# Kernel optimization log

Hardware: AMD Instinct MI355X
Metric: run time of the kernel (lower is better)

Reference implementation:

```python
import jax, jax.numpy as jnp
import numpy as np

S, B, F = 2048, 16, 100
E, H, NOUT, DEC, FF, NH = 512, 512, 10, 1024, 2048, 8
DH = E // NH


def _ln(h, g, b):
    m = h.mean(-1, keepdims=True)
    v = ((h - m) ** 2).mean(-1, keepdims=True)
    return (h - m) * jax.lax.rsqrt(v + 1e-5) * g + b


def setup_inputs() -> dict:
    key = jax.random.key(0)
    ks = jax.random.split(key, 24)
    w = lambda k, shp, s=0.02: (jax.random.normal(k, shp, dtype=jnp.float32) * s)
    return {
        "x": jax.random.normal(ks[0], (S, B, F), dtype=jnp.float32),
        "y": jax.random.normal(ks[1], (S, B), dtype=jnp.float32),
        "enc_W": w(ks[2], (F, E), 0.1), "enc_b": jnp.zeros((E,), jnp.float32),
        "yenc_W": w(ks[3], (1, E), 0.1), "yenc_b": jnp.zeros((E,), jnp.float32),
        "Wq": w(ks[4], (E, E)), "Wk": w(ks[5], (E, E)),
        "Wv": w(ks[6], (E, E)), "Wo": w(ks[7], (E, E)),
        "ln1_g": jnp.ones((E,), jnp.float32), "ln1_b": jnp.zeros((E,), jnp.float32),
        "ln2_g": jnp.ones((E,), jnp.float32), "ln2_b": jnp.zeros((E,), jnp.float32),
        "ffn_W1": w(ks[8], (E, FF)), "ffn_b1": jnp.zeros((FF,), jnp.float32),
        "ffn_W2": w(ks[9], (FF, E)), "ffn_b2": jnp.zeros((E,), jnp.float32),
        "dec_W": w(ks[10], (E, DEC)), "dec_b": jnp.zeros((DEC,), jnp.float32),
        "head_w1_W": w(ks[11], (DEC, F * H)),
        "head_b1_W": w(ks[12], (DEC, H)),
        "head_w2_W": w(ks[13], (DEC, H * NOUT)),
        "head_b2_W": w(ks[14], (DEC, NOUT)),
        "single_eval_pos": 1024,
    }


def reference(x, y, enc_W, enc_b, yenc_W, yenc_b, Wq, Wk, Wv, Wo,
              ln1_g, ln1_b, ln2_g, ln2_b, ffn_W1, ffn_b1, ffn_W2, ffn_b2,
              dec_W, dec_b, head_w1_W, head_b1_W, head_w2_W, head_b2_W,
              single_eval_pos):
    sep = int(single_eval_pos)
    # encoders
    x_src = x @ enc_W + enc_b                       # [S,B,E]
    y_src = y[..., None] @ yenc_W + yenc_b          # [S,B,E]
    train_x = x_src[:sep] + y_src[:sep]             # [T,B,E]

    # inner_forward: one post-LN transformer encoder layer over train tokens
    q = (train_x @ Wq).reshape(sep, B, NH, DH)
    k = (train_x @ Wk).reshape(sep, B, NH, DH)
    v = (train_x @ Wv).reshape(sep, B, NH, DH)
    scores = jnp.einsum('tbhd,sbhd->bhts', q, k) / np.sqrt(DH).astype(np.float32)
    attn = jax.nn.softmax(scores, axis=-1)
    ao = jnp.einsum('bhts,sbhd->tbhd', attn, v).reshape(sep, B, E) @ Wo
    z = _ln(train_x + ao, ln1_g, ln1_b)
    ff = jax.nn.relu(z @ ffn_W1 + ffn_b1) @ ffn_W2 + ffn_b2
    out = _ln(z + ff, ln2_g, ln2_b)                 # [T,B,E]

    # decoder: mean-pool over train tokens, emit per-batch MLP weights
    pooled = out.mean(0)                            # [B,E]
    dh = jax.nn.relu(pooled @ dec_W + dec_b)        # [B,DEC]
    w1 = (dh @ head_w1_W).reshape(B, F, H)
    b1 = dh @ head_b1_W                             # [B,H]
    w2 = (dh @ head_w2_W).reshape(B, H, NOUT)
    b2 = dh @ head_b2_W                             # [B,NOUT]

    # per-batch generated MLP on eval tokens (no_double_embedding path)
    x_eval = jnp.nan_to_num(x[sep:])                # [Eval,B,F]
    h = jnp.einsum('ebf,bfh->ebh', x_eval, w1) + b1
    h = jax.nn.relu(h)
    h = jnp.einsum('ebh,bho->ebo', h, w2) + b2
    return h                                        # [Eval,B,NOUT]
```

## Files before the change

### kernel.cpp

```cpp
#include <hip/hip_runtime.h>
#include <math.h>

#define SEP   1024
#define EVALN 1024
#define BB    16
#define FIN   100
#define FINP  128
#define EE    512
#define NHH   8
#define DHH   64
#define FFNN  2048
#define DECN  1024
#define HHN   512
#define NOUTN 10
#define TBR   (SEP * BB)
#define MB    (1024u * 1024u)

typedef short  s16x8 __attribute__((ext_vector_type(8)));
typedef float  f32x4 __attribute__((ext_vector_type(4)));

__device__ __forceinline__ unsigned short f2b(float f) {
  union { float f; unsigned int u; } v; v.f = f;
  unsigned int u = v.u;
  return (unsigned short)((u + 0x7fffu + ((u >> 16) & 1u)) >> 16);
}

__device__ __forceinline__ float nan2num(float v) {
  if (isnan(v)) return 0.f;
  if (isinf(v)) return v > 0.f ? 3.4028234663852886e38f : -3.4028234663852886e38f;
  return v;
}

__device__ __forceinline__ void gld16(const void* g, void* l) {
  __builtin_amdgcn_global_load_lds(
      (const __attribute__((address_space(1))) unsigned int*)g,
      (__attribute__((address_space(3))) unsigned int*)l, 16, 0, 0);
}

__global__ __launch_bounds__(256)
void transcast(const float* __restrict__ W, unsigned short* __restrict__ Wt,
               int K, int N, int Kp) {
  __shared__ float t[32][33];
  const int n0 = blockIdx.x * 32, k0 = blockIdx.y * 32;
  const int tx = threadIdx.x, ty = threadIdx.y;
#pragma unroll
  for (int r = 0; r < 4; ++r) {
    const int k = k0 + ty + r * 8;
    t[ty + r * 8][tx] = (k < K) ? W[(size_t)k * N + n0 + tx] : 0.f;
  }
  __syncthreads();
#pragma unroll
  for (int r = 0; r < 4; ++r) {
    const int n = n0 + ty + r * 8;
    Wt[(size_t)n * Kp + k0 + tx] = f2b(t[tx][ty + r * 8]);
  }
}

__global__ __launch_bounds__(256)
void castx_kernel(const float* __restrict__ x, unsigned short* __restrict__ xb) {
  const int idx = blockIdx.x * 256 + threadIdx.x;
  const int m = idx >> 7, f = idx & 127;
  xb[idx] = (f < FIN) ? f2b(x[(size_t)m * FIN + f]) : (unsigned short)0;
}

template <bool YENC, bool BIAS, bool RELU, bool OF32, bool OB16>
__global__ __launch_bounds__(256)
void gemm_bf16(const unsigned short* __restrict__ A,
               const unsigned short* __restrict__ Bt,
               float* __restrict__ C32, unsigned short* __restrict__ C16,
               const float* __restrict__ bias, const float* __restrict__ yb2,
               const float* __restrict__ yvec, const float* __restrict__ yW,
               int M, int N, int K) {
  __shared__ unsigned short As[128 * 32];
  __shared__ unsigned short Bs[128 * 32];
  const int tid = threadIdx.x;
  const int wave = tid >> 6, lane = tid & 63;
  const int q = lane >> 4, c = lane & 15;
  const int wm = wave >> 1, wn = wave & 1;
  const int m0 = blockIdx.y * 128, n0 = blockIdx.x * 128;
  const int srow = lane >> 2;
  const int qlog = (lane & 3) ^ (lane >> 4);
  const int rA0 = wave * 32 + srow;
  const int rA1 = rA0 + 16;
  unsigned short* lA0 = As + wave * 1024;
  unsigned short* lA1 = As + wave * 1024 + 512;
  unsigned short* lB0 = Bs + wave * 1024;
  unsigned short* lB1 = Bs + wave * 1024 + 512;
  const unsigned short* gA0 = A + (size_t)(m0 + rA0) * K + qlog * 8;
  const unsigned short* gA1 = A + (size_t)(m0 + rA1) * K + qlog * 8;
  const unsigned short* gB0 = Bt + (size_t)(n0 + rA0) * K + qlog * 8;
  const unsigned short* gB1 = Bt + (size_t)(n0 + rA1) * K + qlog * 8;

  f32x4 acc[4][4];
#pragma unroll
  for (int i = 0; i < 4; ++i)
#pragma unroll
    for (int j = 0; j < 4; ++j) acc[i][j] = (f32x4){0.f, 0.f, 0.f, 0.f};

  const int pchunk = (q ^ (c >> 2)) * 8;
  const int aoff = (wm * 64 + c) * 32 + pchunk;
  const int boff = (wn * 64 + c) * 32 + pchunk;

  for (int k0 = 0; k0 < K; k0 += 32) {
    gld16(gA0 + k0, lA0);
    gld16(gA1 + k0, lA1);
    gld16(gB0 + k0, lB0);
    gld16(gB1 + k0, lB1);
    __syncthreads();
    s16x8 af[4], bf[4];
#pragma unroll
    for (int mi = 0; mi < 4; ++mi)
      af[mi] = *(const s16x8*)&As[aoff + mi * 16 * 32];
#pragma unroll
    for (int ni = 0; ni < 4; ++ni)
      bf[ni] = *(const s16x8*)&Bs[boff + ni * 16 * 32];
#pragma unroll
    for (int mi = 0; mi < 4; ++mi)
#pragma unroll
      for (int ni = 0; ni < 4; ++ni)
        acc[mi][ni] = __builtin_amdgcn_mfma_f32_16x16x32_bf16(
            af[mi], bf[ni], acc[mi][ni], 0, 0, 0);
    __syncthreads();
  }

  float bb[4], yw[4];
#pragma unroll
  for (int ni = 0; ni < 4; ++ni) {
    const int n = n0 + wn * 64 + ni * 16 + c;
    float t = 0.f;
    if (BIAS) t = bias[n];
    if (YENC) t = bias[n] + yb2[n];
    bb[ni] = t;
    yw[ni] = YENC ? yW[n] : 0.f;
  }
#pragma unroll
  for (int mi = 0; mi < 4; ++mi) {
#pragma unroll
    for (int r = 0; r < 4; ++r) {
      const int m = m0 + wm * 64 + mi * 16 + q * 4 + r;
      const float yv = YENC ? yvec[m] : 0.f;
#pragma unroll
      for (int ni = 0; ni < 4; ++ni) {
        const int n = n0 + wn * 64 + ni * 16 + c;
        float val = acc[mi][ni][r] + bb[ni];
        if (YENC) val = fmaf(yv, yw[ni], val);
        if (RELU) val = fmaxf(val, 0.f);
        if (OF32) C32[(size_t)m * N + n] = val;
        if (OB16) C16[(size_t)m * N + n] = f2b(val);
      }
    }
  }
}

__global__ __launch_bounds__(256)
void vtrans(const unsigned short* __restrict__ qkv, unsigned short* __restrict__ vt) {
  __shared__ unsigned short t[64][72];
  const int s0 = blockIdx.x * 64;
  const int h = blockIdx.y, b = blockIdx.z;
  const int tid = threadIdx.x;
  const int r = tid >> 2, o = (tid & 3) * 16;
  const unsigned short* g =
      qkv + ((size_t)(s0 + r) * BB + b) * 1536 + 1024 + h * 64 + o;
  unsigned short tmp[16];
  *(uint4*)tmp = *(const uint4*)g;
  *(uint4*)(tmp + 8) = *(const uint4*)(g + 8);
#pragma unroll
  for (int i = 0; i < 16; ++i) t[o + i][r] = tmp[i];
  __syncthreads();
  unsigned short tmp2[16];
#pragma unroll
  for (int i = 0; i < 16; ++i) {
    const int p = o + i;
    tmp2[i] = t[r][16 * (p & 3) + (p >> 2)];
  }
  unsigned short* out =
      vt + ((size_t)(b * NHH + h) * 64 + r) * 1024 + s0 + o;
  *(uint4*)out = *(const uint4*)&tmp2[0];
  *(uint4*)(out + 8) = *(const uint4*)&tmp2[8];
}

__global__ __launch_bounds__(256)
void attn_mfma(const unsigned short* __restrict__ qkv,
               const unsigned short* __restrict__ vt,
               unsigned short* __restrict__ aob) {
  __shared__ unsigned short Qs[64][72];
  __shared__ unsigned short Ks[64][72];
  __shared__ unsigned short Vts[64][72];
  __shared__ unsigned short Pls[4][16][72];
  const int tid = threadIdx.x;
  const int w = tid >> 6, lane = tid & 63;
  const int q = lane >> 4, c = lane & 15;
  const int hb = blockIdx.x;
  const int h = hb & (NHH - 1), b = hb >> 3;
  const int t0 = blockIdx.y * 64;
  const int bh = b * NHH + h;
  const int sr = tid >> 2, so = (tid & 3) * 16;

  {
    const unsigned short* g =
        qkv + ((size_t)(t0 + sr) * BB + b) * 1536 + h * 64 + so;
    *(uint4*)&Qs[sr][so] = *(const uint4*)g;
    *(uint4*)&Qs[sr][so + 8] = *(const uint4*)(g + 8);
  }
  __syncthreads();
  s16x8 aq[2];
  aq[0] = *(const s16x8*)&Qs[w * 16 + c][q * 8];
  aq[1] = *(const s16x8*)&Qs[w * 16 + c][32 + q * 8];

  float m_s[4], l_s[4];
  f32x4 oacc[4];
#pragma unroll
  for (int r = 0; r < 4; ++r) { m_s[r] = -3.0e38f; l_s[r] = 0.f; }
#pragma unroll
  for (int dt = 0; dt < 4; ++dt) oacc[dt] = (f32x4){0.f, 0.f, 0.f, 0.f};

  uint4 kr0, kr1, vr0, vr1;
  {
    const unsigned short* gk =
        qkv + ((size_t)sr * BB + b) * 1536 + 512 + h * 64 + so;
    kr0 = *(const uint4*)gk; kr1 = *(const uint4*)(gk + 8);
    const unsigned short* gv = vt + ((size_t)bh * 64 + sr) * 1024 + so;
    vr0 = *(const uint4*)gv; vr1 = *(const uint4*)(gv + 8);
  }
  *(uint4*)&Ks[sr][so] = kr0; *(uint4*)&Ks[sr][so + 8] = kr1;
  *(uint4*)&Vts[sr][so] = vr0; *(uint4*)&Vts[sr][so + 8] = vr1;
  __syncthreads();

  for (int s0 = 0; s0 < SEP; s0 += 64) {
    const bool more = (s0 + 64 < SEP);
    if (more) {
      const unsigned short* gk =
          qkv + ((size_t)(s0 + 64 + sr) * BB + b) * 1536 + 512 + h * 64 + so;
      kr0 = *(const uint4*)gk; kr1 = *(const uint4*)(gk + 8);
      const unsigned short* gv =
          vt + ((size_t)bh * 64 + sr) * 1024 + s0 + 64 + so;
      vr0 = *(const uint4*)gv; vr1 = *(const uint4*)(gv + 8);
    }
    f32x4 sacc[4];
#pragma unroll
    for (int ch = 0; ch < 4; ++ch) sacc[ch] = (f32x4){0.f, 0.f, 0.f, 0.f};
#pragma unroll
    for (int ch = 0; ch < 4; ++ch) {
#pragma unroll
      for (int kh = 0; kh < 2; ++kh) {
        s16x8 bk = *(const s16x8*)&Ks[ch * 16 + c][kh * 32 + q * 8];
        sacc[ch] = __builtin_amdgcn_mfma_f32_16x16x32_bf16(
            aq[kh], bk, sacc[ch], 0, 0, 0);
      }
    }
    float rmax[4];
#pragma unroll
    for (int r = 0; r < 4; ++r) {
      float mx = -3.0e38f;
#pragma unroll
      for (int ch = 0; ch < 4; ++ch) mx = fmaxf(mx, sacc[ch][r] * 0.125f);
      rmax[r] = mx;
    }
#pragma unroll
    for (int mask = 1; mask < 16; mask <<= 1)
#pragma unroll
      for (int r = 0; r < 4; ++r)
        rmax[r] = fmaxf(rmax[r], __shfl_xor(rmax[r], mask));
    float alpha[4], rsum[4];
    float p[4][4];
#pragma unroll
    for (int r = 0; r < 4; ++r) {
      const float mnew = fmaxf(m_s[r], rmax[r]);
      alpha[r] = __expf(m_s[r] - mnew);
      float sum = 0.f;
#pragma unroll
      for (int ch = 0; ch < 4; ++ch) {
        const float pv = __expf(sacc[ch][r] * 0.125f - mnew);
        p[ch][r] = pv;
        sum += pv;
      }
      rsum[r] = sum;
      m_s[r] = mnew;
    }
#pragma unroll
    for (int mask = 1; mask < 16; mask <<= 1)
#pragma unroll
      for (int r = 0; r < 4; ++r) rsum[r] += __shfl_xor(rsum[r], mask);
#pragma unroll
    for (int r = 0; r < 4; ++r) l_s[r] = l_s[r] * alpha[r] + rsum[r];
#pragma unroll
    for (int dt = 0; dt < 4; ++dt)
#pragma unroll
      for (int r = 0; r < 4; ++r) oacc[dt][r] *= alpha[r];
#pragma unroll
    for (int r = 0; r < 4; ++r) {
      uint2 pk;
      pk.x = (unsigned)f2b(p[0][r]) | ((unsigned)f2b(p[1][r]) << 16);
      pk.y = (unsigned)f2b(p[2][r]) | ((unsigned)f2b(p[3][r]) << 16);
      *(uint2*)&Pls[w][q * 4 + r][c * 4] = pk;
    }
#pragma unroll
    for (int kh = 0; kh < 2; ++kh) {
      s16x8 ap = *(const s16x8*)&Pls[w][c][kh * 32 + q * 8];
#pragma unroll
      for (int dt = 0; dt < 4; ++dt) {
        s16x8 bv = *(const s16x8*)&Vts[dt * 16 + c][kh * 32 + q * 8];
        oacc[dt] = __builtin_amdgcn_mfma_f32_16x16x32_bf16(
            ap, bv, oacc[dt], 0, 0, 0);
      }
    }
    __syncthreads();
    if (more) {
      *(uint4*)&Ks[sr][so] = kr0; *(uint4*)&Ks[sr][so + 8] = kr1;
      *(uint4*)&Vts[sr][so] = vr0; *(uint4*)&Vts[sr][so + 8] = vr1;
      __syncthreads();
    }
  }
  float inv[4];
#pragma unroll
  for (int r = 0; r < 4; ++r) inv[r] = 1.f / l_s[r];
#pragma unroll
  for (int dt = 0; dt < 4; ++dt) {
#pragma unroll
    for (int r = 0; r < 4; ++r) {
      const int m = t0 + w * 16 + q * 4 + r;
      aob[((size_t)m * BB + b) * EE + h * 64 + dt * 16 + c] =
          f2b(oacc[dt][r] * inv[r]);
    }
  }
}

template <bool B16>
__global__ __launch_bounds__(256)
void ln_k(const float* __restrict__ a, const float* __restrict__ r_,
          const float* __restrict__ g, const float* __restrict__ be,
          float* __restrict__ o32, unsigned short* __restrict__ o16) {
  __shared__ float ss[4], sqs[4];
  const int row = blockIdx.x;
  const int tid = threadIdx.x;
  const size_t base = (size_t)row * EE;
  const float x0 = a[base + tid] + r_[base + tid];
  const float x1 = a[base + tid + 256] + r_[base + tid + 256];
  float s = x0 + x1;
  float sq = x0 * x0 + x1 * x1;
#pragma unroll
  for (int off = 32; off >= 1; off >>= 1) {
    s += __shfl_xor(s, off);
    sq += __shfl_xor(sq, off);
  }
  const int wid = tid >> 6;
  if ((tid & 63) == 0) { ss[wid] = s; sqs[wid] = sq; }
  __syncthreads();
  s = ss[0] + ss[1] + ss[2] + ss[3];
  sq = sqs[0] + sqs[1] + sqs[2] + sqs[3];
  const float mean = s * (1.f / 512.f);
  const float var = sq * (1.f / 512.f) - mean * mean;
  const float rstd = rsqrtf(fmaxf(var, 0.f) + 1e-5f);
  const float v0 = (x0 - mean) * rstd * g[tid] + be[tid];
  const float v1 = (x1 - mean) * rstd * g[tid + 256] + be[tid + 256];
  o32[base + tid] = v0;
  o32[base + tid + 256] = v1;
  if (B16) {
    o16[base + tid] = f2b(v0);
    o16[base + tid + 256] = f2b(v1);
  }
}

__global__ __launch_bounds__(256)
void pool1(const float* __restrict__ outb, float* __restrict__ pp) {
  const int i = blockIdx.x * 256 + threadIdx.x;
  const int ts = blockIdx.y;
  const float* p = outb + (size_t)ts * 64 * (BB * EE) + i;
  float s0 = 0.f, s1 = 0.f, s2 = 0.f, s3 = 0.f;
  for (int t = 0; t < 64; t += 4) {
    s0 += p[(size_t)(t + 0) * (BB * EE)];
    s1 += p[(size_t)(t + 1) * (BB * EE)];
    s2 += p[(size_t)(t + 2) * (BB * EE)];
    s3 += p[(size_t)(t + 3) * (BB * EE)];
  }
  pp[ts * (BB * EE) + i] = (s0 + s1) + (s2 + s3);
}

__global__ __launch_bounds__(256)
void pool2(const float* __restrict__ pp, float* __restrict__ pooled) {
  const int i = blockIdx.x * 256 + threadIdx.x;
  float s = 0.f;
#pragma unroll
  for (int ts = 0; ts < 16; ++ts) s += pp[ts * (BB * EE) + i];
  pooled[i] = s * (1.f / (float)SEP);
}

__global__ __launch_bounds__(256)
void dec1(const float* __restrict__ pooled, const float* __restrict__ dW,
          float* __restrict__ pd) {
  __shared__ float ps[128];
  const int ks = blockIdx.x, b = blockIdx.y;
  const int tid = threadIdx.x;
  if (tid < 128) ps[tid] = pooled[b * EE + ks * 128 + tid];
  __syncthreads();
  const int n = tid * 4;
  float4 acc = {0.f, 0.f, 0.f, 0.f};
  for (int kk = 0; kk < 128; kk += 4) {
    const float4 p4 = *(const float4*)&ps[kk];
#pragma unroll
    for (int i = 0; i < 4; ++i) {
      const float4 w4 = *(const float4*)&dW[(size_t)(ks * 128 + kk + i) * DECN + n];
      const float pv = (i == 0) ? p4.x : (i == 1) ? p4.y : (i == 2) ? p4.z : p4.w;
      acc.x = fmaf(pv, w4.x, acc.x); acc.y = fmaf(pv, w4.y, acc.y);
      acc.z = fmaf(pv, w4.z, acc.z); acc.w = fmaf(pv, w4.w, acc.w);
    }
  }
  *(float4*)&pd[(size_t)(ks * BB + b) * DECN + n] = acc;
}

__global__ __launch_bounds__(256)
void dec2(const float* __restrict__ pd, const float* __restrict__ db,
          float* __restrict__ dh) {
  const int idx = blockIdx.x * 256 + threadIdx.x;
  const int b = idx >> 10, n = idx & 1023;
  float s = db[n];
#pragma unroll
  for (int ks = 0; ks < 4; ++ks) s += pd[(size_t)(ks * BB + b) * DECN + n];
  dh[idx] = fmaxf(s, 0.f);
}

template <int KL>
__global__ __launch_bounds__(256)
void hgemm_split(const float* __restrict__ dh, const float* __restrict__ W,
                 float* __restrict__ part, int N) {
  __shared__ float dhs[16][KL];
  const int tid = threadIdx.x;
  const int n0 = blockIdx.x * 1024;
  const int k0 = blockIdx.y * KL;
  for (int i = tid; i < 16 * (KL / 4); i += 256) {
    const int b = i / (KL / 4), kq = i % (KL / 4);
    *(float4*)&dhs[b][kq * 4] = *(const float4*)&dh[b * DECN + k0 + kq * 4];
  }
  __syncthreads();
  float* pb = part + (size_t)blockIdx.y * 16 * N;
  if ((N & 3) == 0) {
    const int n = n0 + tid * 4;
    if (n + 3 < N) {
      float4 acc[16];
#pragma unroll
      for (int b = 0; b < 16; ++b) acc[b] = (float4){0.f, 0.f, 0.f, 0.f};
      for (int kk = 0; kk < KL; kk += 4) {
        float4 w4[4];
#pragma unroll
        for (int i = 0; i < 4; ++i)
          w4[i] = *(const float4*)&W[(size_t)(k0 + kk + i) * N + n];
#pragma unroll
        for (int b = 0; b < 16; ++b) {
          const float4 d4 = *(const float4*)&dhs[b][kk];
          acc[b].x = fmaf(d4.x, w4[0].x, acc[b].x);
          acc[b].y = fmaf(d4.x, w4[0].y, acc[b].y);
          acc[b].z = fmaf(d4.x, w4[0].z, acc[b].z);
          acc[b].w = fmaf(d4.x, w4[0].w, acc[b].w);
          acc[b].x = fmaf(d4.y, w4[1].x, acc[b].x);
          acc[b].y = fmaf(d4.y, w4[1].y, acc[b].y);
          acc[b].z = fmaf(d4.y, w4[1].z, acc[b].z);
          acc[b].w = fmaf(d4.y, w4[1].w, acc[b].w);
          acc[b].x = fmaf(d4.z, w4[2].x, acc[b].x);
          acc[b].y = fmaf(d4.z, w4[2].y, acc[b].y);
          acc[b].z = fmaf(d4.z, w4[2].z, acc[b].z);
          acc[b].w = fmaf(d4.z, w4[2].w, acc[b].w);
          acc[b].x = fmaf(d4.w, w4[3].x, acc[b].x);
          acc[b].y = fmaf(d4.w, w4[3].y, acc[b].y);
          acc[b].z = fmaf(d4.w, w4[3].z, acc[b].z);
          acc[b].w = fmaf(d4.w, w4[3].w, acc[b].w);
        }
      }
#pragma unroll
      for (int b = 0; b < 16; ++b) *(float4*)&pb[(size_t)b * N + n] = acc[b];
    }
  } else {
    const int n = n0 + tid;
    if (n < N) {
      float acc[16];
#pragma unroll
      for (int b = 0; b < 16; ++b) acc[b] = 0.f;
      for (int kk = 0; kk < KL; ++kk) {
        const float w = W[(size_t)(k0 + kk) * N + n];
#pragma unroll
        for (int b = 0; b < 16; ++b) acc[b] = fmaf(dhs[b][kk], w, acc[b]);
      }
#pragma unroll
      for (int b = 0; b < 16; ++b) pb[(size_t)b * N + n] = acc[b];
    }
  }
}

__global__ __launch_bounds__(256)
void hg_reduce(const float* __restrict__ part, float* __restrict__ out,
               int total, int S) {
  const int i4 = (blockIdx.x * 256 + threadIdx.x) * 4;
  if (i4 >= total) return;
  float4 s = *(const float4*)&part[i4];
  for (int p = 1; p < S; ++p) {
    const float4 v = *(const float4*)&part[(size_t)p * total + i4];
    s.x += v.x; s.y += v.y; s.z += v.z; s.w += v.w;
  }
  *(float4*)&out[i4] = s;
}

__global__ __launch_bounds__(256)
void eval1_kernel(const float* __restrict__ x, const float* __restrict__ w1,
                  const float* __restrict__ b1, float* __restrict__ h1) {
  __shared__ float xs[8][100];
  const int b = blockIdx.z;
  const int e0 = blockIdx.y << 3;
  const int hcol = blockIdx.x * 256 + threadIdx.x;
  for (int i = threadIdx.x; i < 800; i += 256) {
    const int ee = i / 100, f = i - ee * 100;
    xs[ee][f] = nan2num(x[((size_t)(SEP + e0 + ee) * BB + b) * FIN + f]);
  }
  __syncthreads();
  float acc[8];
#pragma unroll
  for (int i = 0; i < 8; ++i) acc[i] = 0.f;
  for (int f = 0; f < FIN; ++f) {
    const float w = w1[(size_t)b * (FIN * HHN) + (size_t)f * HHN + hcol];
#pragma unroll
    for (int ee = 0; ee < 8; ++ee) acc[ee] = fmaf(xs[ee][f], w, acc[ee]);
  }
  const float bias = b1[b * HHN + hcol];
#pragma unroll
  for (int ee = 0; ee < 8; ++ee)
    h1[((size_t)(e0 + ee) * BB + b) * HHN + hcol] = fmaxf(acc[ee] + bias, 0.f);
}

__global__ __launch_bounds__(256)
void eval2_kernel(const float* __restrict__ h1, const float* __restrict__ w2,
                  const float* __restrict__ b2, float* __restrict__ outp) {
  __shared__ float w2s[10][512];
  __shared__ float red[4][64][10];
  const int b = blockIdx.y;
  const int e0 = blockIdx.x * 64;
  const int tid = threadIdx.x;
  const int r = tid & 63, ks = tid >> 6;
  for (int i = tid; i < 5120; i += 256) {
    const int o = i >> 9, k = i & 511;
    w2s[o][k] = w2[(size_t)b * (HHN * NOUTN) + k * NOUTN + o];
  }
  __syncthreads();
  const int eb = (e0 + r) * BB + b;
  const float* hp = h1 + (size_t)eb * HHN + ks * 128;
  float acc[10];
#pragma unroll
  for (int o = 0; o < 10; ++o) acc[o] = 0.f;
  for (int kk = 0; kk < 128; kk += 4) {
    const float4 h4 = *(const float4*)&hp[kk];
#pragma unroll
    for (int o = 0; o < 10; ++o) {
      const float4 w4 = *(const float4*)&w2s[o][ks * 128 + kk];
      acc[o] = fmaf(h4.x, w4.x, acc[o]);
      acc[o] = fmaf(h4.y, w4.y, acc[o]);
      acc[o] = fmaf(h4.z, w4.z, acc[o]);
      acc[o] = fmaf(h4.w, w4.w, acc[o]);
    }
  }
#pragma unroll
  for (int o = 0; o < 10; ++o) red[ks][r][o] = acc[o];
  __syncthreads();
  if (ks == 0) {
#pragma unroll
    for (int o = 0; o < 10; ++o)
      outp[(size_t)eb * NOUTN + o] = red[0][r][o] + red[1][r][o] +
                                     red[2][r][o] + red[3][r][o] +
                                     b2[b * NOUTN + o];
  }
}

extern "C" void kernel_launch(void* const* d_in, const int* in_sizes, int n_in,
                              void* d_out, int out_size, void* d_ws, size_t ws_size,
                              hipStream_t stream) {
  const float* x      = (const float*)d_in[0];
  const float* y      = (const float*)d_in[1];
  const float* enc_W  = (const float*)d_in[2];
  const float* enc_b  = (const float*)d_in[3];
  const float* yenc_W = (const float*)d_in[4];
  const float* yenc_b = (const float*)d_in[5];
  const float* Wq     = (const float*)d_in[6];
  const float* Wk     = (const float*)d_in[7];
  const float* Wv     = (const float*)d_in[8];
  const float* Wo     = (const float*)d_in[9];
  const float* ln1_g  = (const float*)d_in[10];
  const float* ln1_b  = (const float*)d_in[11];
  const float* ln2_g  = (const float*)d_in[12];
  const float* ln2_b  = (const float*)d_in[13];
  const float* ffn_W1 = (const float*)d_in[14];
  const float* ffn_b1 = (const float*)d_in[15];
  const float* ffn_W2 = (const float*)d_in[16];
  const float* ffn_b2 = (const float*)d_in[17];
  const float* dec_W  = (const float*)d_in[18];
  const float* dec_b  = (const float*)d_in[19];
  const float* hw1    = (const float*)d_in[20];
  const float* hb1    = (const float*)d_in[21];
  const float* hw2    = (const float*)d_in[22];
  const float* hb2    = (const float*)d_in[23];

  char* ws = (char*)d_ws;
  unsigned short* ff1b  = (unsigned short*)(ws + 0 * MB);
  unsigned short* xb    = (unsigned short*)(ws + 0 * MB);
  float*          pp    = (float*)(ws + 0 * MB);
  float*          pd    = (float*)(ws + 1 * MB);
  float*          hgp   = (float*)(ws + 2 * MB);
  unsigned short* txb   = (unsigned short*)(ws + 16 * MB);
  unsigned short* vt    = (unsigned short*)(ws + 32 * MB);
  unsigned short* aob   = (unsigned short*)(ws + 48 * MB);
  unsigned short* qkvb  = (unsigned short*)(ws + 64 * MB);
  float*          z32   = (float*)(ws + 64 * MB);
  unsigned short* zb    = (unsigned short*)(ws + 96 * MB);
  float*          tx32  = (float*)(ws + 112 * MB);
  float*          ff2   = (float*)(ws + 112 * MB);
  float*          aop   = (float*)(ws + 144 * MB);
  float*          outb  = (float*)(ws + 144 * MB);
  float*          h1    = (float*)(ws + 144 * MB);
  size_t wo_ = 176 * (size_t)MB;
  unsigned short* WencT = (unsigned short*)(ws + wo_); wo_ += (size_t)EE * FINP * 2;
  unsigned short* WqkvT = (unsigned short*)(ws + wo_); wo_ += (size_t)3 * EE * EE * 2;
  unsigned short* WoT   = (unsigned short*)(ws + wo_); wo_ += (size_t)EE * EE * 2;
  unsigned short* W1T   = (unsigned short*)(ws + wo_); wo_ += (size_t)FFNN * EE * 2;
  unsigned short* W2T   = (unsigned short*)(ws + wo_); wo_ += (size_t)EE * FFNN * 2;
  float* pooled = (float*)(ws + wo_); wo_ += (size_t)BB * EE * 4;
  float* dh     = (float*)(ws + wo_); wo_ += (size_t)BB * DECN * 4;
  float* w1g    = (float*)(ws + wo_); wo_ += (size_t)BB * FIN * HHN * 4;
  float* b1g    = (float*)(ws + wo_); wo_ += (size_t)BB * HHN * 4;
  float* w2g    = (float*)(ws + wo_); wo_ += (size_t)BB * HHN * NOUTN * 4;
  float* b2g    = (float*)(ws + wo_);
  float* outp = (float*)d_out;

  transcast<<<dim3(EE / 32, FINP / 32), dim3(32, 8), 0, stream>>>(enc_W, WencT, FIN, EE, FINP);
  transcast<<<dim3(EE / 32, EE / 32), dim3(32, 8), 0, stream>>>(Wq, WqkvT, EE, EE, EE);
  transcast<<<dim3(EE / 32, EE / 32), dim3(32, 8), 0, stream>>>(Wk, WqkvT + (size_t)EE * EE, EE, EE, EE);
  transcast<<<dim3(EE / 32, EE / 32), dim3(32, 8), 0, stream>>>(Wv, WqkvT + (size_t)2 * EE * EE, EE, EE, EE);
  transcast<<<dim3(EE / 32, EE / 32), dim3(32, 8), 0, stream>>>(Wo, WoT, EE, EE, EE);
  transcast<<<dim3(FFNN / 32, EE / 32), dim3(32, 8), 0, stream>>>(ffn_W1, W1T, EE, FFNN, EE);
  transcast<<<dim3(EE / 32, FFNN / 32), dim3(32, 8), 0, stream>>>(ffn_W2, W2T, FFNN, EE, FFNN);
  castx_kernel<<<(TBR * FINP) / 256, 256, 0, stream>>>(x, xb);

  gemm_bf16<true, false, false, true, true><<<dim3(EE / 128, TBR / 128), 256, 0, stream>>>(
      xb, WencT, tx32, txb, enc_b, yenc_b, y, yenc_W, TBR, EE, FINP);
  gemm_bf16<false, false, false, false, true><<<dim3(1536 / 128, TBR / 128), 256, 0, stream>>>(
      txb, WqkvT, nullptr, qkvb, nullptr, nullptr, nullptr, nullptr, TBR, 1536, EE);
  vtrans<<<dim3(SEP / 64, NHH, BB), 256, 0, stream>>>(qkvb, vt);
  attn_mfma<<<dim3(NHH * BB, SEP / 64), 256, 0, stream>>>(qkvb, vt, aob);
  gemm_bf16<false, false, false, true, false><<<dim3(EE / 128, TBR / 128), 256, 0, stream>>>(
      aob, WoT, aop, nullptr, nullptr, nullptr, nullptr, nullptr, TBR, EE, EE);
  ln_k<true><<<TBR, 256, 0, stream>>>(tx32, aop, ln1_g, ln1_b, z32, zb);
  gemm_bf16<false, true, true, false, true><<<dim3(FFNN / 128, TBR / 128), 256, 0, stream>>>(
      zb, W1T, nullptr, ff1b, ffn_b1, nullptr, nullptr, nullptr, TBR, FFNN, EE);
  gemm_bf16<false, true, false, true, false><<<dim3(EE / 128, TBR / 128), 256, 0, stream>>>(
      ff1b, W2T, ff2, nullptr, ffn_b2, nullptr, nullptr, nullptr, TBR, EE, FFNN);
  ln_k<false><<<TBR, 256, 0, stream>>>(z32, ff2, ln2_g, ln2_b, outb, nullptr);
  pool1<<<dim3(32, 16), 256, 0, stream>>>(outb, pp);
  pool2<<<32, 256, 0, stream>>>(pp, pooled);
  dec1<<<dim3(4, BB), 256, 0, stream>>>(pooled, dec_W, pd);
  dec2<<<64, 256, 0, stream>>>(pd, dec_b, dh);
  hgemm_split<128><<<dim3(50, 8), 256, 0, stream>>>(dh, hw1, hgp, FIN * HHN);
  hg_reduce<<<800, 256, 0, stream>>>(hgp, w1g, BB * FIN * HHN, 8);
  hgemm_split<64><<<dim3(5, 16), 256, 0, stream>>>(dh, hw2, hgp, HHN * NOUTN);
  hg_reduce<<<80, 256, 0, stream>>>(hgp, w2g, BB * HHN * NOUTN, 16);
  hgemm_split<64><<<dim3(1, 16), 256, 0, stream>>>(dh, hb1, hgp, HHN);
  hg_reduce<<<8, 256, 0, stream>>>(hgp, b1g, BB * HHN, 16);
  hgemm_split<64><<<dim3(1, 16), 256, 0, stream>>>(dh, hb2, hgp, NOUTN);
  hg_reduce<<<1, 256, 0, stream>>>(hgp, b2g, BB * NOUTN, 16);
  eval1_kernel<<<dim3(HHN / 256, EVALN / 8, BB), 256, 0, stream>>>(x, w1g, b1g, h1);
  eval2_kernel<<<dim3(EVALN / 64, BB), 256, 0, stream>>>(h1, w2g, b2g, outp);
}
```

Measured before the change: 853.8 us.

## Fuse prep, decoder, small heads and eval kernels; add MFMA priority hints

Merges the eight weight-transpose and input-cast launches into a single prep kernel, and fuses pool2/dec1/dec2 into one decoder kernel. It replaces the b1/b2 head split-GEMMs with one small_heads kernel and fuses the two eval MLP stages so the hidden activations stay in shared memory. It also wraps the attention MFMA blocks with s_setprio. The aim is to cut kernel launch count and intermediate global traffic. The trade-off is less parallelism in some fused kernels, such as dec_fused reading all of K serially and eval_fused using only 160 active threads in its second stage.

Result: no change. 852.8 us (-0.1%).

```diff
diff --git a/kernel.cpp b/kernel.cpp
--- a/kernel.cpp
+++ b/kernel.cpp
@@ -38,29 +38,54 @@
 }
 
 __global__ __launch_bounds__(256)
-void transcast(const float* __restrict__ W, unsigned short* __restrict__ Wt,
-               int K, int N, int Kp) {
-  __shared__ float t[32][33];
-  const int n0 = blockIdx.x * 32, k0 = blockIdx.y * 32;
-  const int tx = threadIdx.x, ty = threadIdx.y;
+void prep_fused(const float* __restrict__ x,
+                const float* __restrict__ enc_W, const float* __restrict__ Wq,
+                const float* __restrict__ Wk, const float* __restrict__ Wv,
+                const float* __restrict__ Wo, const float* __restrict__ W1,
+                const float* __restrict__ W2,
+                unsigned short* __restrict__ xb, unsigned short* __restrict__ WencT,
+                unsigned short* __restrict__ WqkvT, unsigned short* __restrict__ WoT,
+                unsigned short* __restrict__ W1T, unsigned short* __restrict__ W2T) {
+  const int bid = blockIdx.x;
+  const int tid = threadIdx.x;
+  if (bid < 8192) {
+    const int idx = bid * 256 + tid;
+    const int m = idx >> 7, f = idx & 127;
+    xb[idx] = (f < FIN) ? f2b(x[(size_t)m * FIN + f]) : (unsigned short)0;
+    return;
+  }
+  int t = bid - 8192;
+  const float* W; unsigned short* Wt; int K, N, Kp, gx;
+  if (t < 64) {
+    W = enc_W; Wt = WencT; K = FIN; N = EE; Kp = FINP; gx = 16;
+  } else if ((t -= 64) < 256) {
+    W = Wq; Wt = WqkvT; K = EE; N = EE; Kp = EE; gx = 16;
+  } else if ((t -= 256) < 256) {
+    W = Wk; Wt = WqkvT + (size_t)EE * EE; K = EE; N = EE; Kp = EE; gx = 16;
+  } else if ((t -= 256) < 256) {
+    W = Wv; Wt = WqkvT + (size_t)2 * EE * EE; K = EE; N = EE; Kp = EE; gx = 16;
+  } else if ((t -= 256) < 256) {
+    W = Wo; Wt = WoT; K = EE; N = EE; Kp = EE; gx = 16;
+  } else if ((t -= 256) < 1024) {
+    W = W1; Wt = W1T; K = EE; N = FFNN; Kp = EE; gx = 64;
+  } else {
+    t -= 1024;
+    W = W2; Wt = W2T; K = FFNN; N = EE; Kp = FFNN; gx = 16;
+  }
+  __shared__ float tb[32][33];
+  const int n0 = (t % gx) * 32, k0 = (t / gx) * 32;
+  const int tx = tid & 31, ty = tid >> 5;
 #pragma unroll
   for (int r = 0; r < 4; ++r) {
     const int k = k0 + ty + r * 8;
-    t[ty + r * 8][tx] = (k < K) ? W[(size_t)k * N + n0 + tx] : 0.f;
+    tb[ty + r * 8][tx] = (k < K) ? W[(size_t)k * N + n0 + tx] : 0.f;
   }
   __syncthreads();
 #pragma unroll
   for (int r = 0; r < 4; ++r) {
     const int n = n0 + ty + r * 8;
-    Wt[(size_t)n * Kp + k0 + tx] = f2b(t[tx][ty + r * 8]);
-  }
-}
-
-__global__ __launch_bounds__(256)
-void castx_kernel(const float* __restrict__ x, unsigned short* __restrict__ xb) {
-  const int idx = blockIdx.x * 256 + threadIdx.x;
-  const int m = idx >> 7, f = idx & 127;
-  xb[idx] = (f < FIN) ? f2b(x[(size_t)m * FIN + f]) : (unsigned short)0;
+    Wt[(size_t)n * Kp + k0 + tx] = f2b(tb[tx][ty + r * 8]);
+  }
 }
 
 template <bool YENC, bool BIAS, bool RELU, bool OF32, bool OB16>
@@ -239,6 +264,7 @@
     f32x4 sacc[4];
 #pragma unroll
     for (int ch = 0; ch < 4; ++ch) sacc[ch] = (f32x4){0.f, 0.f, 0.f, 0.f};
+    __builtin_amdgcn_s_setprio(1);
 #pragma unroll
     for (int ch = 0; ch < 4; ++ch) {
 #pragma unroll
@@ -248,6 +274,7 @@
             aq[kh], bk, sacc[ch], 0, 0, 0);
       }
     }
+    __builtin_amdgcn_s_setprio(0);
     float rmax[4];
 #pragma unroll
     for (int r = 0; r < 4; ++r) {
@@ -294,6 +321,7 @@
       pk.y = (unsigned)f2b(p[2][r]) | ((unsigned)f2b(p[3][r]) << 16);
       *(uint2*)&Pls[w][q * 4 + r][c * 4] = pk;
     }
+    __builtin_amdgcn_s_setprio(1);
 #pragma unroll
     for (int kh = 0; kh < 2; ++kh) {
       s16x8 ap = *(const s16x8*)&Pls[w][c][kh * 32 + q * 8];
@@ -304,6 +332,7 @@
             ap, bv, oacc[dt], 0, 0, 0);
       }
     }
+    __builtin_amdgcn_s_setprio(0);
     __syncthreads();
     if (more) {
       *(uint4*)&Ks[sr][so] = kr0; *(uint4*)&Ks[sr][so + 8] = kr1;
@@ -377,46 +406,27 @@
 }
 
 __global__ __launch_bounds__(256)
-void pool2(const float* __restrict__ pp, float* __restrict__ pooled) {
-  const int i = blockIdx.x * 256 + threadIdx.x;
-  float s = 0.f;
-#pragma unroll
-  for (int ts = 0; ts < 16; ++ts) s += pp[ts * (BB * EE) + i];
-  pooled[i] = s * (1.f / (float)SEP);
-}
-
-__global__ __launch_bounds__(256)
-void dec1(const float* __restrict__ pooled, const float* __restrict__ dW,
-          float* __restrict__ pd) {
-  __shared__ float ps[128];
-  const int ks = blockIdx.x, b = blockIdx.y;
-  const int tid = threadIdx.x;
-  if (tid < 128) ps[tid] = pooled[b * EE + ks * 128 + tid];
-  __syncthreads();
-  const int n = tid * 4;
-  float4 acc = {0.f, 0.f, 0.f, 0.f};
-  for (int kk = 0; kk < 128; kk += 4) {
-    const float4 p4 = *(const float4*)&ps[kk];
-#pragma unroll
-    for (int i = 0; i < 4; ++i) {
-      const float4 w4 = *(const float4*)&dW[(size_t)(ks * 128 + kk + i) * DECN + n];
-      const float pv = (i == 0) ? p4.x : (i == 1) ? p4.y : (i == 2) ? p4.z : p4.w;
-      acc.x = fmaf(pv, w4.x, acc.x); acc.y = fmaf(pv, w4.y, acc.y);
-      acc.z = fmaf(pv, w4.z, acc.z); acc.w = fmaf(pv, w4.w, acc.w);
-    }
-  }
-  *(float4*)&pd[(size_t)(ks * BB + b) * DECN + n] = acc;
-}
-
-__global__ __launch_bounds__(256)
-void dec2(const float* __restrict__ pd, const float* __restrict__ db,
-          float* __restrict__ dh) {
-  const int idx = blockIdx.x * 256 + threadIdx.x;
-  const int b = idx >> 10, n = idx & 1023;
-  float s = db[n];
-#pragma unroll
-  for (int ks = 0; ks < 4; ++ks) s += pd[(size_t)(ks * BB + b) * DECN + n];
-  dh[idx] = fmaxf(s, 0.f);
+void dec_fused(const float* __restrict__ pp, const float* __restrict__ dW,
+               const float* __restrict__ db, float* __restrict__ dh) {
+  __shared__ float ps[EE];
+  const int b = blockIdx.y;
+  const int n = blockIdx.x * 256 + threadIdx.x;
+  for (int i = threadIdx.x; i < EE; i += 256) {
+    float s = 0.f;
+#pragma unroll
+    for (int ts = 0; ts < 16; ++ts) s += pp[ts * (BB * EE) + b * EE + i];
+    ps[i] = s * (1.f / (float)SEP);
+  }
+  __syncthreads();
+  float a0 = db[n], a1 = 0.f, a2 = 0.f, a3 = 0.f;
+  for (int k = 0; k < EE; k += 4) {
+    const float4 p4 = *(const float4*)&ps[k];
+    a0 = fmaf(p4.x, dW[(size_t)(k + 0) * DECN + n], a0);
+    a1 = fmaf(p4.y, dW[(size_t)(k + 1) * DECN + n], a1);
+    a2 = fmaf(p4.z, dW[(size_t)(k + 2) * DECN + n], a2);
+    a3 = fmaf(p4.w, dW[(size_t)(k + 3) * DECN + n], a3);
+  }
+  dh[b * DECN + n] = fmaxf((a0 + a1) + (a2 + a3), 0.f);
 }
 
 template <int KL>
@@ -499,70 +509,107 @@
 }
 
 __global__ __launch_bounds__(256)
-void eval1_kernel(const float* __restrict__ x, const float* __restrict__ w1,
-                  const float* __restrict__ b1, float* __restrict__ h1) {
+void small_heads(const float* __restrict__ dh, const float* __restrict__ hb1W,
+                 const float* __restrict__ hb2W, float* __restrict__ b1g,
+                 float* __restrict__ b2g) {
+  __shared__ float ds[DECN];
+  __shared__ float red2[16][NOUTN];
+  const int b = blockIdx.y;
+  const int tid = threadIdx.x;
+  for (int i = tid; i < DECN; i += 256) ds[i] = dh[b * DECN + i];
+  __syncthreads();
+  if (blockIdx.x == 0) {
+#pragma unroll
+    for (int pass = 0; pass < 2; ++pass) {
+      const int n = tid + pass * 256;
+      float a0 = 0.f, a1 = 0.f, a2 = 0.f, a3 = 0.f;
+      for (int k = 0; k < DECN; k += 4) {
+        a0 = fmaf(ds[k + 0], hb1W[(size_t)(k + 0) * HHN + n], a0);
+        a1 = fmaf(ds[k + 1], hb1W[(size_t)(k + 1) * HHN + n], a1);
+        a2 = fmaf(ds[k + 2], hb1W[(size_t)(k + 2) * HHN + n], a2);
+        a3 = fmaf(ds[k + 3], hb1W[(size_t)(k + 3) * HHN + n], a3);
+      }
+      b1g[b * HHN + n] = (a0 + a1) + (a2 + a3);
+    }
+  } else {
+    if (tid < 160) {
+      const int o = tid % NOUTN, ks = tid / NOUTN;
+      float a0 = 0.f, a1 = 0.f;
+      const int kb = ks * 64;
+      for (int k = 0; k < 64; k += 2) {
+        a0 = fmaf(ds[kb + k + 0], hb2W[(size_t)(kb + k + 0) * NOUTN + o], a0);
+        a1 = fmaf(ds[kb + k + 1], hb2W[(size_t)(kb + k + 1) * NOUTN + o], a1);
+      }
+      red2[ks][o] = a0 + a1;
+    }
+    __syncthreads();
+    if (tid < NOUTN) {
+      float s = 0.f;
+#pragma unroll
+      for (int ks = 0; ks < 16; ++ks) s += red2[ks][tid];
+      b2g[b * NOUTN + tid] = s;
+    }
+  }
+}
+
+__global__ __launch_bounds__(256)
+void eval_fused(const float* __restrict__ x, const float* __restrict__ w1,
+                const float* __restrict__ b1, const float* __restrict__ w2,
+                const float* __restrict__ b2, float* __restrict__ outp) {
   __shared__ float xs[8][100];
-  const int b = blockIdx.z;
-  const int e0 = blockIdx.y << 3;
-  const int hcol = blockIdx.x * 256 + threadIdx.x;
-  for (int i = threadIdx.x; i < 800; i += 256) {
+  __shared__ float w2s[HHN][NOUTN];
+  __shared__ float hs[8][516];
+  __shared__ float red[2][80];
+  const int b = blockIdx.y;
+  const int e0 = blockIdx.x << 3;
+  const int tid = threadIdx.x;
+  for (int i = tid; i < 800; i += 256) {
     const int ee = i / 100, f = i - ee * 100;
     xs[ee][f] = nan2num(x[((size_t)(SEP + e0 + ee) * BB + b) * FIN + f]);
   }
-  __syncthreads();
-  float acc[8];
-#pragma unroll
-  for (int i = 0; i < 8; ++i) acc[i] = 0.f;
+  for (int i = tid; i < HHN * NOUTN; i += 256)
+    ((float*)w2s)[i] = w2[(size_t)b * (HHN * NOUTN) + i];
+  __syncthreads();
+  const float bb0 = b1[b * HHN + tid];
+  const float bb1 = b1[b * HHN + tid + 256];
+  float a0[8], a1[8];
+#pragma unroll
+  for (int ee = 0; ee < 8; ++ee) { a0[ee] = 0.f; a1[ee] = 0.f; }
   for (int f = 0; f < FIN; ++f) {
-    const float w = w1[(size_t)b * (FIN * HHN) + (size_t)f * HHN + hcol];
-#pragma unroll
-    for (int ee = 0; ee < 8; ++ee) acc[ee] = fmaf(xs[ee][f], w, acc[ee]);
-  }
-  const float bias = b1[b * HHN + hcol];
-#pragma unroll
-  for (int ee = 0; ee < 8; ++ee)
-    h1[((size_t)(e0 + ee) * BB + b) * HHN + hcol] = fmaxf(acc[ee] + bias, 0.f);
-}
-
-__global__ __launch_bounds__(256)
-void eval2_kernel(const float* __restrict__ h1, const float* __restrict__ w2,
-                  const float* __restrict__ b2, float* __restrict__ outp) {
-  __shared__ float w2s[10][512];
-  __shared__ float red[4][64][10];
-  const int b = blockIdx.y;
-  const int e0 = blockIdx.x * 64;
-  const int tid = threadIdx.x;
-  const int r = tid & 63, ks = tid >> 6;
-  for (int i = tid; i < 5120; i += 256) {
-    const int o = i >> 9, k = i & 511;
-    w2s[o][k] = w2[(size_t)b * (HHN * NOUTN) + k * NOUTN + o];
-  }
-  __syncthreads();
-  const int eb = (e0 + r) * BB + b;
-  const float* hp = h1 + (size_t)eb * HHN + ks * 128;
-  float acc[10];
-#pragma unroll
-  for (int o = 0; o < 10; ++o) acc[o] = 0.f;
-  for (int kk = 0; kk < 128; kk += 4) {
-    const float4 h4 = *(const float4*)&hp[kk];
-#pragma unroll
-    for (int o = 0; o < 10; ++o) {
-      const float4 w4 = *(const float4*)&w2s[o][ks * 128 + kk];
-      acc[o] = fmaf(h4.x, w4.x, acc[o]);
-      acc[o] = fmaf(h4.y, w4.y, acc[o]);
-      acc[o] = fmaf(h4.z, w4.z, acc[o]);
-      acc[o] = fmaf(h4.w, w4.w, acc[o]);
-    }
-  }
-#pragma unroll
-  for (int o = 0; o < 10; ++o) red[ks][r][o] = acc[o];
-  __syncthreads();
-  if (ks == 0) {
-#pragma unroll
-    for (int o = 0; o < 10; ++o)
-      outp[(size_t)eb * NOUTN + o] = red[0][r][o] + red[1][r][o] +
-                                     red[2][r][o] + red[3][r][o] +
-                                     b2[b * NOUTN + o];
+    const float w0 = w1[(size_t)b * (FIN * HHN) + (size_t)f * HHN + tid];
+    const float w8 = w1[(size_t)b * (FIN * HHN) + (size_t)f * HHN + tid + 256];
+#pragma unroll
+    for (int ee = 0; ee < 8; ++ee) {
+      a0[ee] = fmaf(xs[ee][f], w0, a0[ee]);
+      a1[ee] = fmaf(xs[ee][f], w8, a1[ee]);
+    }
+  }
+#pragma unroll
+  for (int ee = 0; ee < 8; ++ee) {
+    hs[ee][tid]       = fmaxf(a0[ee] + bb0, 0.f);
+    hs[ee][tid + 256] = fmaxf(a1[ee] + bb1, 0.f);
+  }
+  __syncthreads();
+  if (tid < 160) {
+    const int o = tid % NOUTN;
+    const int ee = (tid / NOUTN) % 8;
+    const int ks = tid / 80;
+    const float* hp = &hs[ee][ks * 256];
+    const float* wp = (const float*)w2s + (size_t)ks * 256 * NOUTN + o;
+    float c0 = 0.f, c1 = 0.f, c2 = 0.f, c3 = 0.f;
+    for (int k = 0; k < 256; k += 4) {
+      c0 = fmaf(hp[k + 0], wp[(k + 0) * NOUTN], c0);
+      c1 = fmaf(hp[k + 1], wp[(k + 1) * NOUTN], c1);
+      c2 = fmaf(hp[k + 2], wp[(k + 2) * NOUTN], c2);
+      c3 = fmaf(hp[k + 3], wp[(k + 3) * NOUTN], c3);
+    }
+    red[ks][ee * NOUTN + o] = (c0 + c1) + (c2 + c3);
+  }
+  __syncthreads();
+  if (tid < 80) {
+    const int o = tid % NOUTN, ee = tid / NOUTN;
+    outp[((size_t)(e0 + ee) * BB + b) * NOUTN + o] =
+        red[0][tid] + red[1][tid] + b2[b * NOUTN + o];
   }
 }
 
@@ -598,7 +645,6 @@
   unsigned short* ff1b  = (unsigned short*)(ws + 0 * MB);
   unsigned short* xb    = (unsigned short*)(ws + 0 * MB);
   float*          pp    = (float*)(ws + 0 * MB);
-  float*          pd    = (float*)(ws + 1 * MB);
   float*          hgp   = (float*)(ws + 2 * MB);
   unsigned short* txb   = (unsigned short*)(ws + 16 * MB);
   unsigned short* vt    = (unsigned short*)(ws + 32 * MB);
@@ -610,14 +656,12 @@
   float*          ff2   = (float*)(ws + 112 * MB);
   float*          aop   = (float*)(ws + 144 * MB);
   float*          outb  = (float*)(ws + 144 * MB);
-  float*          h1    = (float*)(ws + 144 * MB);
   size_t wo_ = 176 * (size_t)MB;
   unsigned short* WencT = (unsigned short*)(ws + wo_); wo_ += (size_t)EE * FINP * 2;
   unsigned short* WqkvT = (unsigned short*)(ws + wo_); wo_ += (size_t)3 * EE * EE * 2;
   unsigned short* WoT   = (unsigned short*)(ws + wo_); wo_ += (size_t)EE * EE * 2;
   unsigned short* W1T   = (unsigned short*)(ws + wo_); wo_ += (size_t)FFNN * EE * 2;
   unsigned short* W2T   = (unsigned short*)(ws + wo_); wo_ += (size_t)EE * FFNN * 2;
-  float* pooled = (float*)(ws + wo_); wo_ += (size_t)BB * EE * 4;
   float* dh     = (float*)(ws + wo_); wo_ += (size_t)BB * DECN * 4;
   float* w1g    = (float*)(ws + wo_); wo_ += (size_t)BB * FIN * HHN * 4;
   float* b1g    = (float*)(ws + wo_); wo_ += (size_t)BB * HHN * 4;
@@ -625,14 +669,9 @@
   float* b2g    = (float*)(ws + wo_);
   float* outp = (float*)d_out;
 
-  transcast<<<dim3(EE / 32, FINP / 32), dim3(32, 8), 0, stream>>>(enc_W, WencT, FIN, EE, FINP);
-  transcast<<<dim3(EE / 32, EE / 32), dim3(32, 8), 0, stream>>>(Wq, WqkvT, EE, EE, EE);
-  transcast<<<dim3(EE / 32, EE / 32), dim3(32, 8), 0, stream>>>(Wk, WqkvT + (size_t)EE * EE, EE, EE, EE);
-  transcast<<<dim3(EE / 32, EE / 32), dim3(32, 8), 0, stream>>>(Wv, WqkvT + (size_t)2 * EE * EE, EE, EE, EE);
-  transcast<<<dim3(EE / 32, EE / 32), dim3(32, 8), 0, stream>>>(Wo, WoT, EE, EE, EE);
-  transcast<<<dim3(FFNN / 32, EE / 32), dim3(32, 8), 0, stream>>>(ffn_W1, W1T, EE, FFNN, EE);
-  transcast<<<dim3(EE / 32, FFNN / 32), dim3(32, 8), 0, stream>>>(ffn_W2, W2T, FFNN, EE, FFNN);
-  castx_kernel<<<(TBR * FINP) / 256, 256, 0, stream>>>(x, xb);
+  prep_fused<<<8192 + 64 + 4 * 256 + 1024 + 1024, 256, 0, stream>>>(
+      x, enc_W, Wq, Wk, Wv, Wo, ffn_W1, ffn_W2,
+      xb, WencT, WqkvT, WoT, W1T, W2T);
 
   gemm_bf16<true, false, false, true, true><<<dim3(EE / 128, TBR / 128), 256, 0, stream>>>(
       xb, WencT, tx32, txb, enc_b, yenc_b, y, yenc_W, TBR, EE, FINP);
@@ -649,17 +688,11 @@
       ff1b, W2T, ff2, nullptr, ffn_b2, nullptr, nullptr, nullptr, TBR, EE, FFNN);
   ln_k<false><<<TBR, 256, 0, stream>>>(z32, ff2, ln2_g, ln2_b, outb, nullptr);
   pool1<<<dim3(32, 16), 256, 0, stream>>>(outb, pp);
-  pool2<<<32, 256, 0, stream>>>(pp, pooled);
-  dec1<<<dim3(4, BB), 256, 0, stream>>>(pooled, dec_W, pd);
-  dec2<<<64, 256, 0, stream>>>(pd, dec_b, dh);
+  dec_fused<<<dim3(DECN / 256, BB), 256, 0, stream>>>(pp, dec_W, dec_b, dh);
   hgemm_split<128><<<dim3(50, 8), 256, 0, stream>>>(dh, hw1, hgp, FIN * HHN);
   hg_reduce<<<800, 256, 0, stream>>>(hgp, w1g, BB * FIN * HHN, 8);
   hgemm_split<64><<<dim3(5, 16), 256, 0, stream>>>(dh, hw2, hgp, HHN * NOUTN);
   hg_reduce<<<80, 256, 0, stream>>>(hgp, w2g, BB * HHN * NOUTN, 16);
-  hgemm_split<64><<<dim3(1, 16), 256, 0, stream>>>(dh, hb1, hgp, HHN);
-  hg_reduce<<<8, 256, 0, stream>>>(hgp, b1g, BB * HHN, 16);
-  hgemm_split<64><<<dim3(1, 16), 256, 0, stream>>>(dh, hb2, hgp, NOUTN);
-  hg_reduce<<<1, 256, 0, stream>>>(hgp, b2g, BB * NOUTN, 16);
-  eval1_kernel<<<dim3(HHN / 256, EVALN / 8, BB), 256, 0, stream>>>(x, w1g, b1g, h1);
-  eval2_kernel<<<dim3(EVALN / 64, BB), 256, 0, stream>>>(h1, w2g, b2g, outp);
-}
+  small_heads<<<dim3(2, BB), 256, 0, stream>>>(dh, hb1, hb2, b1g, b2g);
+  eval_fused<<<dim3(EVALN / 8, BB), 256, 0, stream>>>(x, w1g, b1g, w2g, b2g, outp);
+}
```
